# Kernel tuning notes

Hardware: AMD Instinct MI355X
Metric: run time of the kernel (lower is better)

Reference implementation:

```python
import jax, jax.numpy as jnp
import numpy as np

BATCH = 4096
IN_DIM = 512
OUT_DIM = 512
GRID_SIZE = 5
K = 3


def _extended_grid():
    # Original: grid = linspace(-1, 1, grid_size+1), spacing h = 2/grid_size.
    # The de Boor-Cox recursion in the source indexes up to grid[grid_size+2k],
    # so we extend the uniform grid to the right with the same spacing.
    h = 2.0 / GRID_SIZE
    return (-1.0 + h * jnp.arange(GRID_SIZE + 2 * K + 1)).astype(jnp.float32)


def bspline_basis(x, grid, k):
    """Vectorized de Boor-Cox recursion.
    x: [..., ] floats; returns basis [..., grid_size + k].
    Identical math to the recursive b_spline_basis in the source, but computed
    bottom-up over all knot intervals at once (no redundant recomputation).
    """
    xe = x[..., None]  # [..., 1]
    # degree-0: indicator of half-open knot intervals, [..., n_knots-1]
    B = ((grid[:-1] <= xe) & (xe < grid[1:])).astype(x.dtype)
    for d in range(1, k + 1):
        n = grid.shape[0] - d - 1
        gi, gid = grid[:n], grid[d:d + n]          # grid[i], grid[i+d]
        gi1, gid1 = grid[1:n + 1], grid[d + 1:d + n + 1]  # grid[i+1], grid[i+d+1]
        # uniform grid -> denominators are d*h, never zero
        B = (xe - gi) / (gid - gi) * B[..., :n] + (gid1 - xe) / (gid1 - gi1) * B[..., 1:n + 1]
    return B  # [..., grid_size + k]


def setup_inputs() -> dict:
    key = jax.random.key(0)
    k1, k2 = jax.random.split(key)
    x = jax.random.uniform(k1, (BATCH, IN_DIM), jnp.float32) * 2.0 - 1.0  # in [-1, 1)
    spline_coeff = jax.random.normal(k2, (IN_DIM, OUT_DIM, GRID_SIZE + K), jnp.float32)
    spline_scaling = jnp.ones((IN_DIM, OUT_DIM), jnp.float32)
    return {"x": x, "spline_coeff": spline_coeff, "spline_scaling": spline_scaling}


def reference(x, spline_coeff, spline_scaling):
    grid = _extended_grid()
    basis = bspline_basis(x, grid, K)  # [B, in_dim, grid_size+k]
    # out[b, j] = sum_i scaling[i,j] * sum_g basis[b,i,g] * coeff[i,j,g]
    return jnp.einsum('big,ijg,ij->bj', basis, spline_coeff, spline_scaling)
```

## Files before the change

### kernel.cpp

```cpp
#include <hip/hip_runtime.h>
#include <hip/hip_bf16.h>
#include <stdint.h>


#define BATCH   4096
#define IN_DIM  512
#define OUT_DIM 512
#define KDIM    (IN_DIM * 8)
#define NKT     (KDIM / 64)

typedef short short8 __attribute__((ext_vector_type(8)));
typedef float f32x4  __attribute__((ext_vector_type(4)));

#define WAIT_VM8 0xF78
#define WAIT_VM4 0xF74
#define WAIT_VM0 0xF70

__device__ __forceinline__ unsigned short f2bf(float f) {
  union { float f; unsigned int u; } v; v.f = f;
  unsigned int r = v.u + 0x7FFFu + ((v.u >> 16) & 1u);
  return (unsigned short)(r >> 16);
}

__device__ __forceinline__ void bspline_win(float xv, float* w, int* mm) {
  float t = (xv + 1.0f) * 2.5f;
  int m = (int)t;
  m = m < 0 ? 0 : (m > 4 ? 4 : m);
  float u  = t - (float)m;
  float u2 = u * u, u3 = u2 * u, om = 1.0f - u;
  w[0] = om * om * om * (1.0f / 6.0f);
  w[1] = (3.0f * u3 - 6.0f * u2 + 4.0f) * (1.0f / 6.0f);
  w[2] = (-3.0f * u3 + 3.0f * u2 + 3.0f * u + 1.0f) * (1.0f / 6.0f);
  w[3] = u3 * (1.0f / 6.0f);
  *mm = m;
}

__device__ __forceinline__ short8 basis_pack8(float xv) {
  float w[4]; int m;
  bspline_win(xv, w, &m);
  short8 h = {};
#pragma unroll
  for (int g = 0; g < 8; ++g) {
    int d = g - m + 3;
    float v = (d == 0) ? w[0] : (d == 1) ? w[1] : (d == 2) ? w[2] : (d == 3) ? w[3] : 0.0f;
    h[g] = (short)f2bf(v);
  }
  return h;
}

__device__ __forceinline__ void async_load16(const void* g, void* l) {
  __builtin_amdgcn_global_load_lds(
      (__attribute__((address_space(1))) void*)(uintptr_t)g,
      (__attribute__((address_space(3))) void*)(unsigned int)(uintptr_t)l,
      16, 0, 0);
}

__global__ void kan_prep(const float* __restrict__ x,
                         const float* __restrict__ coeff,
                         const float* __restrict__ scaling,
                         unsigned short* __restrict__ Ag,
                         unsigned short* __restrict__ Wt) {
  const int b = blockIdx.x;
  if (b < (BATCH * IN_DIM) / 256) {
    int idx = b * 256 + threadIdx.x;
    short8 h = basis_pack8(x[idx]);
    *reinterpret_cast<short8*>(Ag + (size_t)idx * 8) = h;
  } else {
    int idx = (b - (BATCH * IN_DIM) / 256) * 256 + threadIdx.x;
    int i = idx >> 9, j = idx & 511;
    float s = scaling[idx];
    const float4* cp = reinterpret_cast<const float4*>(coeff) + (size_t)idx * 2;
    float4 c0 = cp[0], c1 = cp[1];
    short8 h;
    h[0] = (short)f2bf(c0.x * s); h[1] = (short)f2bf(c0.y * s);
    h[2] = (short)f2bf(c0.z * s); h[3] = (short)f2bf(c0.w * s);
    h[4] = (short)f2bf(c1.x * s); h[5] = (short)f2bf(c1.y * s);
    h[6] = (short)f2bf(c1.z * s); h[7] = (short)f2bf(c1.w * s);
    *reinterpret_cast<short8*>(Wt + (size_t)j * KDIM + i * 8) = h;
  }
}

__global__ __launch_bounds__(256, 2)
void kan_gemm_p(const unsigned short* __restrict__ Ag,
                const unsigned short* __restrict__ Wt,
                float* __restrict__ out) {
  __shared__ unsigned short As[3][64 * 64];
  __shared__ unsigned short Bs[3][64 * 64];

  const int tid  = threadIdx.x;
  const int lane = tid & 63;
  const int wid  = tid >> 6;
  const int wm = wid >> 1, wn = wid & 1;
  const int ln = lane & 15, quad = lane >> 4;

  const int b    = blockIdx.x;
  const int row0 = (b & 63) * 64;
  const int col0 = (b >> 6) * 64;

  f32x4 acc[2][2] = {};

  const int lr = lane >> 3;
  const int cg = (lane & 7) ^ lr;

  const unsigned short* aRow = Ag + (size_t)(row0 + wid * 16 + lr) * KDIM + cg * 8;
  const unsigned short* bRow = Wt + (size_t)(col0 + wid * 16 + lr) * KDIM + cg * 8;

  auto issue = [&](int kt, int st) {
    const int k0 = kt * 64;
#pragma unroll
    for (int t = 0; t < 2; ++t) {
      const int rbase = wid * 16 + t * 8;
      async_load16(aRow + (size_t)t * 8 * KDIM + k0, &As[st][rbase * 64]);
      async_load16(bRow + (size_t)t * 8 * KDIM + k0, &Bs[st][rbase * 64]);
    }
  };

  auto compute = [&](int st) {
#pragma unroll
    for (int kk = 0; kk < 2; ++kk) {
      short8 af[2], bfr[2];
#pragma unroll
      for (int mt = 0; mt < 2; ++mt) {
        const int r    = wm * 32 + mt * 16 + ln;
        const int slot = (kk * 4 + quad) ^ (r & 7);
        af[mt] = *reinterpret_cast<const short8*>(&As[st][r * 64 + slot * 8]);
      }
#pragma unroll
      for (int nt = 0; nt < 2; ++nt) {
        const int c    = wn * 32 + nt * 16 + ln;
        const int slot = (kk * 4 + quad) ^ (c & 7);
        bfr[nt] = *reinterpret_cast<const short8*>(&Bs[st][c * 64 + slot * 8]);
      }
#pragma unroll
      for (int mt = 0; mt < 2; ++mt)
#pragma unroll
        for (int nt = 0; nt < 2; ++nt)
          acc[mt][nt] = __builtin_amdgcn_mfma_f32_16x16x32_bf16(af[mt], bfr[nt], acc[mt][nt], 0, 0, 0);
    }
  };

  issue(0, 0); issue(1, 1); issue(2, 2);

  int st = 0;
  for (int kt = 0; kt < NKT - 3; ++kt) {
    __builtin_amdgcn_s_waitcnt(WAIT_VM8);
    __builtin_amdgcn_s_barrier();
    compute(st);
    __builtin_amdgcn_s_barrier();
    issue(kt + 3, st);
    st = (st == 2) ? 0 : st + 1;
  }
  __builtin_amdgcn_s_waitcnt(WAIT_VM8);
  __builtin_amdgcn_s_barrier();
  compute(st);
  st = (st == 2) ? 0 : st + 1;
  __builtin_amdgcn_s_waitcnt(WAIT_VM4);
  __builtin_amdgcn_s_barrier();
  compute(st);
  st = (st == 2) ? 0 : st + 1;
  __builtin_amdgcn_s_waitcnt(WAIT_VM0);
  __builtin_amdgcn_s_barrier();
  compute(st);

#pragma unroll
  for (int mt = 0; mt < 2; ++mt)
#pragma unroll
    for (int nt = 0; nt < 2; ++nt) {
      const int col = col0 + wn * 32 + nt * 16 + ln;
#pragma unroll
      for (int r = 0; r < 4; ++r) {
        const int row = row0 + wm * 32 + mt * 16 + quad * 4 + r;
        out[(size_t)row * OUT_DIM + col] = acc[mt][nt][r];
      }
    }
}

__global__ __launch_bounds__(256, 2)
void kan_gemm_fb(const float* __restrict__ x, const float* __restrict__ coeff,
                 const float* __restrict__ scaling, float* __restrict__ out) {
  __shared__ unsigned short As[64 * 64];
  __shared__ unsigned short Bs[64 * 64];

  const int tid  = threadIdx.x;
  const int lane = tid & 63;
  const int wid  = tid >> 6;
  const int wm = wid >> 1, wn = wid & 1;
  const int ln = lane & 15, quad = lane >> 4;
  const int row0 = blockIdx.y * 64;
  const int col0 = blockIdx.x * 64;

  f32x4 acc[2][2] = {};

  for (int kt = 0; kt < KDIM / 64; ++kt) {
#pragma unroll
    for (int pp = 0; pp < 2; ++pp) {
      const int p  = tid + pp * 256;
      const int rn = p & 63;
      const int il = p >> 6;
      const int sw = ((il ^ (rn & 7)) * 8);
      short8 ha = basis_pack8(x[(size_t)(row0 + rn) * IN_DIM + kt * 8 + il]);
      *reinterpret_cast<short8*>(&As[rn * 64 + sw]) = ha;
      const float* cbase = coeff + (size_t)(kt * 8 + il) * 4096 + (size_t)(col0 + rn) * 8;
      float4 c0 = reinterpret_cast<const float4*>(cbase)[0];
      float4 c1 = reinterpret_cast<const float4*>(cbase)[1];
      float s = scaling[(size_t)(kt * 8 + il) * OUT_DIM + col0 + rn];
      short8 hb;
      hb[0] = (short)f2bf(c0.x * s); hb[1] = (short)f2bf(c0.y * s);
      hb[2] = (short)f2bf(c0.z * s); hb[3] = (short)f2bf(c0.w * s);
      hb[4] = (short)f2bf(c1.x * s); hb[5] = (short)f2bf(c1.y * s);
      hb[6] = (short)f2bf(c1.z * s); hb[7] = (short)f2bf(c1.w * s);
      *reinterpret_cast<short8*>(&Bs[rn * 64 + sw]) = hb;
    }
    __syncthreads();
#pragma unroll
    for (int kk = 0; kk < 2; ++kk) {
      short8 af[2], bfr[2];
#pragma unroll
      for (int mt = 0; mt < 2; ++mt) {
        const int r  = wm * 32 + mt * 16 + ln;
        const int pc = (kk * 4 + quad) ^ (r & 7);
        af[mt] = *reinterpret_cast<const short8*>(&As[r * 64 + pc * 8]);
      }
#pragma unroll
      for (int nt = 0; nt < 2; ++nt) {
        const int c  = wn * 32 + nt * 16 + ln;
        const int pc = (kk * 4 + quad) ^ (c & 7);
        bfr[nt] = *reinterpret_cast<const short8*>(&Bs[c * 64 + pc * 8]);
      }
#pragma unroll
      for (int mt = 0; mt < 2; ++mt)
#pragma unroll
        for (int nt = 0; nt < 2; ++nt)
          acc[mt][nt] = __builtin_amdgcn_mfma_f32_16x16x32_bf16(af[mt], bfr[nt], acc[mt][nt], 0, 0, 0);
    }
    __syncthreads();
  }
#pragma unroll
  for (int mt = 0; mt < 2; ++mt)
#pragma unroll
    for (int nt = 0; nt < 2; ++nt) {
      const int col = col0 + wn * 32 + nt * 16 + ln;
#pragma unroll
      for (int r = 0; r < 4; ++r) {
        const int row = row0 + wm * 32 + mt * 16 + quad * 4 + r;
        out[(size_t)row * OUT_DIM + col] = acc[mt][nt][r];
      }
    }
}

extern "C" void kernel_launch(void* const* d_in, const int* in_sizes, int n_in,
                              void* d_out, int out_size, void* d_ws, size_t ws_size,
                              hipStream_t stream) {
  const float* x       = (const float*)d_in[0];
  const float* coeff   = (const float*)d_in[1];
  const float* scaling = (const float*)d_in[2];
  float* out = (float*)d_out;

  const size_t needA = (size_t)BATCH * KDIM * 2;
  const size_t needW = (size_t)OUT_DIM * KDIM * 2;

  if (ws_size >= needA + needW) {
    unsigned short* Ag = (unsigned short*)d_ws;
    unsigned short* Wt = (unsigned short*)((char*)d_ws + needA);
    kan_prep<<<(BATCH * IN_DIM) / 256 + (IN_DIM * OUT_DIM) / 256, 256, 0, stream>>>(
        x, coeff, scaling, Ag, Wt);
    kan_gemm_p<<<(BATCH / 64) * (OUT_DIM / 64), 256, 0, stream>>>(Ag, Wt, out);
  } else {
    kan_gemm_fb<<<dim3(OUT_DIM / 64, BATCH / 64), 256, 0, stream>>>(x, coeff, scaling, out);
  }
}
```

Measured before the change: 99.50 us.

## Fuse B-spline basis expansion into GEMM, loading raw x instead of prebuilt A

```diff
diff --git a/kernel.cpp b/kernel.cpp
--- a/kernel.cpp
+++ b/kernel.cpp
@@ -55,37 +55,36 @@
       16, 0, 0);
 }
 
-__global__ void kan_prep(const float* __restrict__ x,
-                         const float* __restrict__ coeff,
-                         const float* __restrict__ scaling,
-                         unsigned short* __restrict__ Ag,
-                         unsigned short* __restrict__ Wt) {
-  const int b = blockIdx.x;
-  if (b < (BATCH * IN_DIM) / 256) {
-    int idx = b * 256 + threadIdx.x;
-    short8 h = basis_pack8(x[idx]);
-    *reinterpret_cast<short8*>(Ag + (size_t)idx * 8) = h;
-  } else {
-    int idx = (b - (BATCH * IN_DIM) / 256) * 256 + threadIdx.x;
-    int i = idx >> 9, j = idx & 511;
-    float s = scaling[idx];
-    const float4* cp = reinterpret_cast<const float4*>(coeff) + (size_t)idx * 2;
-    float4 c0 = cp[0], c1 = cp[1];
-    short8 h;
-    h[0] = (short)f2bf(c0.x * s); h[1] = (short)f2bf(c0.y * s);
-    h[2] = (short)f2bf(c0.z * s); h[3] = (short)f2bf(c0.w * s);
-    h[4] = (short)f2bf(c1.x * s); h[5] = (short)f2bf(c1.y * s);
-    h[6] = (short)f2bf(c1.z * s); h[7] = (short)f2bf(c1.w * s);
-    *reinterpret_cast<short8*>(Wt + (size_t)j * KDIM + i * 8) = h;
-  }
+__device__ __forceinline__ void async_load4(const void* g, void* l) {
+  __builtin_amdgcn_global_load_lds(
+      (__attribute__((address_space(1))) void*)(uintptr_t)g,
+      (__attribute__((address_space(3))) void*)(unsigned int)(uintptr_t)l,
+      4, 0, 0);
+}
+
+__global__ void kan_prep_w(const float* __restrict__ coeff,
+                           const float* __restrict__ scaling,
+                           unsigned short* __restrict__ Wt) {
+  int idx = blockIdx.x * 256 + threadIdx.x;
+  int i = idx >> 9, j = idx & 511;
+  float s = scaling[idx];
+  const float4* cp = reinterpret_cast<const float4*>(coeff) + (size_t)idx * 2;
+  float4 c0 = cp[0], c1 = cp[1];
+  short8 h;
+  h[0] = (short)f2bf(c0.x * s); h[1] = (short)f2bf(c0.y * s);
+  h[2] = (short)f2bf(c0.z * s); h[3] = (short)f2bf(c0.w * s);
+  h[4] = (short)f2bf(c1.x * s); h[5] = (short)f2bf(c1.y * s);
+  h[6] = (short)f2bf(c1.z * s); h[7] = (short)f2bf(c1.w * s);
+  *reinterpret_cast<short8*>(Wt + (size_t)j * KDIM + i * 8) = h;
 }
 
 __global__ __launch_bounds__(256, 2)
-void kan_gemm_p(const unsigned short* __restrict__ Ag,
+void kan_gemm_f(const float* __restrict__ x,
                 const unsigned short* __restrict__ Wt,
                 float* __restrict__ out) {
-  __shared__ unsigned short As[3][64 * 64];
+  __shared__ unsigned short As[2][64 * 64];
   __shared__ unsigned short Bs[3][64 * 64];
+  __shared__ float          xs[3][64 * 8];
 
   const int tid  = threadIdx.x;
   const int lane = tid & 63;
@@ -102,20 +101,35 @@
   const int lr = lane >> 3;
   const int cg = (lane & 7) ^ lr;
 
-  const unsigned short* aRow = Ag + (size_t)(row0 + wid * 16 + lr) * KDIM + cg * 8;
   const unsigned short* bRow = Wt + (size_t)(col0 + wid * 16 + lr) * KDIM + cg * 8;
+  const float* xSrc = x + (size_t)(row0 + wid * 16 + (lane >> 3)) * IN_DIM + (lane & 7);
 
   auto issue = [&](int kt, int st) {
     const int k0 = kt * 64;
 #pragma unroll
     for (int t = 0; t < 2; ++t) {
       const int rbase = wid * 16 + t * 8;
-      async_load16(aRow + (size_t)t * 8 * KDIM + k0, &As[st][rbase * 64]);
       async_load16(bRow + (size_t)t * 8 * KDIM + k0, &Bs[st][rbase * 64]);
     }
+#pragma unroll
+    for (int t = 0; t < 2; ++t) {
+      async_load4(xSrc + (size_t)t * 8 * IN_DIM + kt * 8, &xs[st][wid * 128 + t * 64]);
+    }
   };
 
-  auto compute = [&](int st) {
+  auto stageA = [&](int kt) {
+    const int sx = kt % 3, sa = kt & 1;
+#pragma unroll
+    for (int h2 = 0; h2 < 2; ++h2) {
+      const int q  = tid + h2 * 256;
+      const int rn = q >> 3, il = q & 7;
+      float xv = xs[sx][q];
+      short8 hh = basis_pack8(xv);
+      *reinterpret_cast<short8*>(&As[sa][rn * 64 + ((il ^ (rn & 7)) * 8)]) = hh;
+    }
+  };
+
+  auto compute = [&](int sa, int sb) {
 #pragma unroll
     for (int kk = 0; kk < 2; ++kk) {
       short8 af[2], bfr[2];
@@ -123,13 +137,13 @@
       for (int mt = 0; mt < 2; ++mt) {
         const int r    = wm * 32 + mt * 16 + ln;
         const int slot = (kk * 4 + quad) ^ (r & 7);
-        af[mt] = *reinterpret_cast<const short8*>(&As[st][r * 64 + slot * 8]);
+        af[mt] = *reinterpret_cast<const short8*>(&As[sa][r * 64 + slot * 8]);
       }
 #pragma unroll
       for (int nt = 0; nt < 2; ++nt) {
         const int c    = wn * 32 + nt * 16 + ln;
         const int slot = (kk * 4 + quad) ^ (c & 7);
-        bfr[nt] = *reinterpret_cast<const short8*>(&Bs[st][c * 64 + slot * 8]);
+        bfr[nt] = *reinterpret_cast<const short8*>(&Bs[sb][c * 64 + slot * 8]);
       }
 #pragma unroll
       for (int mt = 0; mt < 2; ++mt)
@@ -141,26 +155,44 @@
 
   issue(0, 0); issue(1, 1); issue(2, 2);
 
-  int st = 0;
   for (int kt = 0; kt < NKT - 3; ++kt) {
+    const int sb = kt % 3;
     __builtin_amdgcn_s_waitcnt(WAIT_VM8);
     __builtin_amdgcn_s_barrier();
-    compute(st);
-    __builtin_amdgcn_s_barrier();
-    issue(kt + 3, st);
-    st = (st == 2) ? 0 : st + 1;
-  }
-  __builtin_amdgcn_s_waitcnt(WAIT_VM8);
-  __builtin_amdgcn_s_barrier();
-  compute(st);
-  st = (st == 2) ? 0 : st + 1;
-  __builtin_amdgcn_s_waitcnt(WAIT_VM4);
-  __builtin_amdgcn_s_barrier();
-  compute(st);
-  st = (st == 2) ? 0 : st + 1;
-  __builtin_amdgcn_s_waitcnt(WAIT_VM0);
-  __builtin_amdgcn_s_barrier();
-  compute(st);
+    stageA(kt);
+    asm volatile("s_waitcnt lgkmcnt(0)" ::: "memory");
+    __builtin_amdgcn_s_barrier();
+    compute(kt & 1, sb);
+    __builtin_amdgcn_s_barrier();
+    issue(kt + 3, sb);
+  }
+  {
+    int kt = NKT - 3;
+    __builtin_amdgcn_s_waitcnt(WAIT_VM8);
+    __builtin_amdgcn_s_barrier();
+    stageA(kt);
+    asm volatile("s_waitcnt lgkmcnt(0)" ::: "memory");
+    __builtin_amdgcn_s_barrier();
+    compute(kt & 1, kt % 3);
+  }
+  {
+    int kt = NKT - 2;
+    __builtin_amdgcn_s_waitcnt(WAIT_VM4);
+    __builtin_amdgcn_s_barrier();
+    stageA(kt);
+    asm volatile("s_waitcnt lgkmcnt(0)" ::: "memory");
+    __builtin_amdgcn_s_barrier();
+    compute(kt & 1, kt % 3);
+  }
+  {
+    int kt = NKT - 1;
+    __builtin_amdgcn_s_waitcnt(WAIT_VM0);
+    __builtin_amdgcn_s_barrier();
+    stageA(kt);
+    asm volatile("s_waitcnt lgkmcnt(0)" ::: "memory");
+    __builtin_amdgcn_s_barrier();
+    compute(kt & 1, kt % 3);
+  }
 
 #pragma unroll
   for (int mt = 0; mt < 2; ++mt)
@@ -256,15 +288,12 @@
   const float* scaling = (const float*)d_in[2];
   float* out = (float*)d_out;
 
-  const size_t needA = (size_t)BATCH * KDIM * 2;
   const size_t needW = (size_t)OUT_DIM * KDIM * 2;
 
-  if (ws_size >= needA + needW) {
-    unsigned short* Ag = (unsigned short*)d_ws;
-    unsigned short* Wt = (unsigned short*)((char*)d_ws + needA);
-    kan_prep<<<(BATCH * IN_DIM) / 256 + (IN_DIM * OUT_DIM) / 256, 256, 0, stream>>>(
-        x, coeff, scaling, Ag, Wt);
-    kan_gemm_p<<<(BATCH / 64) * (OUT_DIM / 64), 256, 0, stream>>>(Ag, Wt, out);
+  if (ws_size >= needW) {
+    unsigned short* Wt = (unsigned short*)d_ws;
+    kan_prep_w<<<(IN_DIM * OUT_DIM) / 256, 256, 0, stream>>>(coeff, scaling, Wt);
+    kan_gemm_f<<<(BATCH / 64) * (OUT_DIM / 64), 256, 0, stream>>>(x, Wt, out);
   } else {
     kan_gemm_fb<<<dim3(OUT_DIM / 64, BATCH / 64), 256, 0, stream>>>(x, coeff, scaling, out);
   }
```

After: 146.7 us. +47.4%, slower.

## Use 128x128 tiles with split-K across four slices and a reduction kernel

Applied to the files above, without the earlier changes.

```diff
diff --git a/kernel.cpp b/kernel.cpp
--- a/kernel.cpp
+++ b/kernel.cpp
@@ -7,13 +7,14 @@
 #define IN_DIM  512
 #define OUT_DIM 512
 #define KDIM    (IN_DIM * 8)
-#define NKT     (KDIM / 64)
+#define SPLITK  4
+#define KSPAN   (KDIM / SPLITK)
+#define NKS     (KSPAN / 64)
 
 typedef short short8 __attribute__((ext_vector_type(8)));
 typedef float f32x4  __attribute__((ext_vector_type(4)));
 
 #define WAIT_VM8 0xF78
-#define WAIT_VM4 0xF74
 #define WAIT_VM0 0xF70
 
 __device__ __forceinline__ unsigned short f2bf(float f) {
@@ -81,11 +82,11 @@
 }
 
 __global__ __launch_bounds__(256, 2)
-void kan_gemm_p(const unsigned short* __restrict__ Ag,
+void kan_gemm_s(const unsigned short* __restrict__ Ag,
                 const unsigned short* __restrict__ Wt,
-                float* __restrict__ out) {
-  __shared__ unsigned short As[3][64 * 64];
-  __shared__ unsigned short Bs[3][64 * 64];
+                float* __restrict__ Pt) {
+  __shared__ unsigned short As[2][128 * 64];
+  __shared__ unsigned short Bs[2][128 * 64];
 
   const int tid  = threadIdx.x;
   const int lane = tid & 63;
@@ -94,85 +95,94 @@
   const int ln = lane & 15, quad = lane >> 4;
 
   const int b    = blockIdx.x;
-  const int row0 = (b & 63) * 64;
-  const int col0 = (b >> 6) * 64;
-
-  f32x4 acc[2][2] = {};
+  const int ks   = b & 3;
+  const int mt   = (b >> 2) & 31;
+  const int nt   = b >> 7;
+  const int row0 = mt * 128;
+  const int col0 = nt * 128;
+  const int k0   = ks * KSPAN;
+
+  f32x4 acc[4][4] = {};
 
   const int lr = lane >> 3;
   const int cg = (lane & 7) ^ lr;
 
-  const unsigned short* aRow = Ag + (size_t)(row0 + wid * 16 + lr) * KDIM + cg * 8;
-  const unsigned short* bRow = Wt + (size_t)(col0 + wid * 16 + lr) * KDIM + cg * 8;
+  const unsigned short* aRow = Ag + (size_t)(row0 + wid * 32 + lr) * KDIM + k0 + cg * 8;
+  const unsigned short* bRow = Wt + (size_t)(col0 + wid * 32 + lr) * KDIM + k0 + cg * 8;
 
   auto issue = [&](int kt, int st) {
-    const int k0 = kt * 64;
-#pragma unroll
-    for (int t = 0; t < 2; ++t) {
-      const int rbase = wid * 16 + t * 8;
-      async_load16(aRow + (size_t)t * 8 * KDIM + k0, &As[st][rbase * 64]);
-      async_load16(bRow + (size_t)t * 8 * KDIM + k0, &Bs[st][rbase * 64]);
+    const int kk0 = kt * 64;
+#pragma unroll
+    for (int t = 0; t < 4; ++t) {
+      const int rbase = wid * 32 + t * 8;
+      async_load16(aRow + (size_t)t * 8 * KDIM + kk0, &As[st][rbase * 64]);
+      async_load16(bRow + (size_t)t * 8 * KDIM + kk0, &Bs[st][rbase * 64]);
     }
   };
 
   auto compute = [&](int st) {
 #pragma unroll
     for (int kk = 0; kk < 2; ++kk) {
-      short8 af[2], bfr[2];
-#pragma unroll
-      for (int mt = 0; mt < 2; ++mt) {
-        const int r    = wm * 32 + mt * 16 + ln;
+      short8 af[4], bfr[4];
+#pragma unroll
+      for (int m = 0; m < 4; ++m) {
+        const int r    = wm * 64 + m * 16 + ln;
         const int slot = (kk * 4 + quad) ^ (r & 7);
-        af[mt] = *reinterpret_cast<const short8*>(&As[st][r * 64 + slot * 8]);
-      }
-#pragma unroll
-      for (int nt = 0; nt < 2; ++nt) {
-        const int c    = wn * 32 + nt * 16 + ln;
+        af[m] = *reinterpret_cast<const short8*>(&As[st][r * 64 + slot * 8]);
+      }
+#pragma unroll
+      for (int n = 0; n < 4; ++n) {
+        const int c    = wn * 64 + n * 16 + ln;
         const int slot = (kk * 4 + quad) ^ (c & 7);
-        bfr[nt] = *reinterpret_cast<const short8*>(&Bs[st][c * 64 + slot * 8]);
-      }
-#pragma unroll
-      for (int mt = 0; mt < 2; ++mt)
-#pragma unroll
-        for (int nt = 0; nt < 2; ++nt)
-          acc[mt][nt] = __builtin_amdgcn_mfma_f32_16x16x32_bf16(af[mt], bfr[nt], acc[mt][nt], 0, 0, 0);
+        bfr[n] = *reinterpret_cast<const short8*>(&Bs[st][c * 64 + slot * 8]);
+      }
+#pragma unroll
+      for (int m = 0; m < 4; ++m)
+#pragma unroll
+        for (int n = 0; n < 4; ++n)
+          acc[m][n] = __builtin_amdgcn_mfma_f32_16x16x32_bf16(af[m], bfr[n], acc[m][n], 0, 0, 0);
     }
   };
 
-  issue(0, 0); issue(1, 1); issue(2, 2);
-
-  int st = 0;
-  for (int kt = 0; kt < NKT - 3; ++kt) {
+  issue(0, 0); issue(1, 1);
+
+  for (int kt = 0; kt < NKS - 1; ++kt) {
     __builtin_amdgcn_s_waitcnt(WAIT_VM8);
     __builtin_amdgcn_s_barrier();
-    compute(st);
+    compute(kt & 1);
     __builtin_amdgcn_s_barrier();
-    issue(kt + 3, st);
-    st = (st == 2) ? 0 : st + 1;
-  }
-  __builtin_amdgcn_s_waitcnt(WAIT_VM8);
-  __builtin_amdgcn_s_barrier();
-  compute(st);
-  st = (st == 2) ? 0 : st + 1;
-  __builtin_amdgcn_s_waitcnt(WAIT_VM4);
-  __builtin_amdgcn_s_barrier();
-  compute(st);
-  st = (st == 2) ? 0 : st + 1;
+    if (kt + 2 < NKS) issue(kt + 2, kt & 1);
+  }
   __builtin_amdgcn_s_waitcnt(WAIT_VM0);
   __builtin_amdgcn_s_barrier();
-  compute(st);
-
-#pragma unroll
-  for (int mt = 0; mt < 2; ++mt)
-#pragma unroll
-    for (int nt = 0; nt < 2; ++nt) {
-      const int col = col0 + wn * 32 + nt * 16 + ln;
+  compute((NKS - 1) & 1);
+
+  float* P = Pt + (size_t)ks * BATCH * OUT_DIM;
+#pragma unroll
+  for (int m = 0; m < 4; ++m)
+#pragma unroll
+    for (int n = 0; n < 4; ++n) {
+      const int col = col0 + wn * 64 + n * 16 + ln;
 #pragma unroll
       for (int r = 0; r < 4; ++r) {
-        const int row = row0 + wm * 32 + mt * 16 + quad * 4 + r;
-        out[(size_t)row * OUT_DIM + col] = acc[mt][nt][r];
-      }
-    }
+        const int row = row0 + wm * 64 + m * 16 + quad * 4 + r;
+        P[(size_t)row * OUT_DIM + col] = acc[m][n][r];
+      }
+    }
+}
+
+__global__ __launch_bounds__(256)
+void kan_reduce(const float* __restrict__ Pt, float* __restrict__ out) {
+  const size_t Q = (size_t)BATCH * OUT_DIM / 4;
+  const size_t t = (size_t)blockIdx.x * 256 + threadIdx.x;
+  const float4* p = reinterpret_cast<const float4*>(Pt);
+  float4 a = p[t], b = p[t + Q], c = p[t + 2 * Q], d = p[t + 3 * Q];
+  float4 s;
+  s.x = (a.x + b.x) + (c.x + d.x);
+  s.y = (a.y + b.y) + (c.y + d.y);
+  s.z = (a.z + b.z) + (c.z + d.z);
+  s.w = (a.w + b.w) + (c.w + d.w);
+  reinterpret_cast<float4*>(out)[t] = s;
 }
 
 __global__ __launch_bounds__(256, 2)
@@ -256,15 +266,18 @@
   const float* scaling = (const float*)d_in[2];
   float* out = (float*)d_out;
 
-  const size_t needA = (size_t)BATCH * KDIM * 2;
-  const size_t needW = (size_t)OUT_DIM * KDIM * 2;
-
-  if (ws_size >= needA + needW) {
+  const size_t offW = (size_t)BATCH * KDIM * 2;
+  const size_t offP = offW + (size_t)OUT_DIM * KDIM * 2;
+  const size_t need = offP + (size_t)SPLITK * BATCH * OUT_DIM * 4;
+
+  if (ws_size >= need) {
     unsigned short* Ag = (unsigned short*)d_ws;
-    unsigned short* Wt = (unsigned short*)((char*)d_ws + needA);
+    unsigned short* Wt = (unsigned short*)((char*)d_ws + offW);
+    float*          Pt = (float*)((char*)d_ws + offP);
     kan_prep<<<(BATCH * IN_DIM) / 256 + (IN_DIM * OUT_DIM) / 256, 256, 0, stream>>>(
         x, coeff, scaling, Ag, Wt);
-    kan_gemm_p<<<(BATCH / 64) * (OUT_DIM / 64), 256, 0, stream>>>(Ag, Wt, out);
+    kan_gemm_s<<<(BATCH / 128) * (OUT_DIM / 128) * SPLITK, 256, 0, stream>>>(Ag, Wt, Pt);
+    kan_reduce<<<(BATCH * OUT_DIM / 4) / 256, 256, 0, stream>>>(Pt, out);
   } else {
     kan_gemm_fb<<<dim3(OUT_DIM / 64, BATCH / 64), 256, 0, stream>>>(x, coeff, scaling, out);
   }
```

Result: no change. 100.4 us (+0.9%).
